# Kernel tuning notes

Hardware: AMD Instinct MI355X
Metric: run time of the kernel (lower is better)

Reference implementation:

```python
import jax, jax.numpy as jnp
import numpy as np

N, E, D, D_OUT = 100000, 3200000, 64, 64
EPS = 1e-5


def setup_inputs() -> dict:
    key = jax.random.key(0)
    ks = jax.random.split(key, 16)
    s = 1.0 / np.sqrt(D)
    inp = {
        "x": jax.random.normal(ks[0], (N, D), dtype=jnp.float32),
        "edge_index": jax.random.randint(ks[1], (2, E), 0, N, dtype=jnp.int64),
        # layer 1: GCNConv weight/bias, fc weight/bias, BN gamma/beta
        "W1": jax.random.uniform(ks[2], (D, D), jnp.float32, -s, s),
        "b1": jnp.zeros((D,), jnp.float32),
        "fw1": jax.random.uniform(ks[3], (D, D), jnp.float32, -s, s),
        "fb1": jax.random.uniform(ks[4], (D,), jnp.float32, -s, s),
        "g1": jnp.ones((D,), jnp.float32),
        "bt1": jnp.zeros((D,), jnp.float32),
        # layer 2
        "W2": jax.random.uniform(ks[5], (D, D), jnp.float32, -s, s),
        "b2": jnp.zeros((D,), jnp.float32),
        "fw2": jax.random.uniform(ks[6], (D, D_OUT), jnp.float32, -s, s),
        "fb2": jax.random.uniform(ks[7], (D_OUT,), jnp.float32, -s, s),
        "g2": jnp.ones((D_OUT,), jnp.float32),
        "bt2": jnp.zeros((D_OUT,), jnp.float32),
    }
    return inp


def _gcn_conv(x, W, b, src, dst, dinv):
    # x' = X W, then symmetric-normalized scatter-add aggregation (self loops included)
    h = x @ W                                   # [N, D]
    msg = (dinv[src] * dinv[dst])[:, None] * h[src]  # [E+N, D]
    out = jax.ops.segment_sum(msg, dst, num_segments=N)
    return out + b


def _fc_bn_relu(x, fw, fb, g, bt):
    y = x @ fw + fb
    mu = jnp.mean(y, axis=0)
    var = jnp.mean((y - mu) ** 2, axis=0)  # biased var (torch BN training mode)
    y = (y - mu) * jax.lax.rsqrt(var + EPS) * g + bt
    return jax.nn.relu(y)


def reference(x, edge_index, W1, b1, fw1, fb1, g1, bt1, W2, b2, fw2, fb2, g2, bt2):
    loop = jnp.arange(N, dtype=edge_index.dtype)
    src = jnp.concatenate([edge_index[0], loop])  # add self loops
    dst = jnp.concatenate([edge_index[1], loop])
    deg = jax.ops.segment_sum(jnp.ones_like(dst, dtype=x.dtype), dst, num_segments=N)
    dinv = jax.lax.rsqrt(deg)  # deg >= 1 thanks to self loops

    h = _gcn_conv(x, W1, b1, src, dst, dinv)
    h = _fc_bn_relu(h, fw1, fb1, g1, bt1)
    h = _gcn_conv(h, W2, b2, src, dst, dinv)
    h = _fc_bn_relu(h, fw2, fb2, g2, bt2)
    return h
```

## Files before the change

### kernel.cpp

```cpp
#include <hip/hip_runtime.h>

#define N_NODES 100000
#define N_EDGES 3200000
#define D 64
#define EPS 1e-5f

#define BSHIFT 7
#define BNODES 128
#define NBUCK ((N_NODES + BNODES - 1) / BNODES)
#define P1_CHUNK 4096
#define NB_P1 ((N_EDGES + P1_CHUNK - 1) / P1_CHUNK)
#define SRC_MASK 0x1FFFFu
#define BCAP 4480
#define TBL_STRIDE 784

typedef _Float16 f16x8 __attribute__((ext_vector_type(8)));
typedef _Float16 half2v __attribute__((ext_vector_type(2)));
typedef unsigned int u32x4 __attribute__((ext_vector_type(4)));
typedef __attribute__((ext_vector_type(4))) float f32x4;

__device__ __forceinline__ unsigned short f2h(float f) {
  return __builtin_bit_cast(unsigned short, (_Float16)f);
}
__device__ __forceinline__ half2v u2h(unsigned int u) {
  return __builtin_bit_cast(half2v, u);
}
__device__ __forceinline__ unsigned int h2u(half2v h) {
  return __builtin_bit_cast(unsigned int, h);
}
__device__ __forceinline__ float2 hpair(unsigned int u) {
  half2v h = __builtin_bit_cast(half2v, u);
  return make_float2((float)h.x, (float)h.y);
}
__device__ __forceinline__ void addp(half2v a[4], uint4 u) {
  a[0] += u2h(u.x);
  a[1] += u2h(u.y);
  a[2] += u2h(u.z);
  a[3] += u2h(u.w);
}

__global__ __launch_bounds__(256) void combine_weights(
    const float* __restrict__ W1, const float* __restrict__ b1,
    const float* __restrict__ fw1, const float* __restrict__ fb1,
    const float* __restrict__ W2, const float* __restrict__ b2,
    const float* __restrict__ fw2, const float* __restrict__ fb2,
    unsigned int* __restrict__ WcB1, float* __restrict__ bc1,
    unsigned int* __restrict__ WcB2, float* __restrict__ bc2,
    float* __restrict__ stats) {
  if (blockIdx.x == 2) {
    if (threadIdx.x < 256) stats[threadIdx.x] = 0.0f;
    return;
  }
  const float* W  = blockIdx.x ? W2  : W1;
  const float* fw = blockIdx.x ? fw2 : fw1;
  const float* b  = blockIdx.x ? b2  : b1;
  const float* fb = blockIdx.x ? fb2 : fb1;
  unsigned int* WcB = blockIdx.x ? WcB2 : WcB1;
  float* bc = blockIdx.x ? bc2 : bc1;

  __shared__ float sW[64 * 64];
  __shared__ float sf[64 * 64];
  __shared__ float sC[64 * 64];
  for (int i = threadIdx.x; i < 4096; i += 256) { sW[i] = W[i]; sf[i] = fw[i]; }
  __syncthreads();
  for (int o = threadIdx.x; o < 4096; o += 256) {
    int i = o >> 6, j = o & 63;
    float acc = 0.f;
    #pragma unroll
    for (int k = 0; k < 64; ++k) acc += sW[i * 64 + k] * sf[k * 64 + j];
    sC[o] = acc;
  }
  __syncthreads();
  for (int o = threadIdx.x; o < 2048; o += 256) {
    int jj = o & 3, L = (o >> 2) & 63, kh = (o >> 8) & 1, nt = o >> 9;
    int k0 = (L >> 4) * 8 + jj * 2 + kh * 32;
    int n  = nt * 16 + (L & 15);
    unsigned int lo = f2h(sC[k0 * 64 + n]);
    unsigned int hi = f2h(sC[(k0 + 1) * 64 + n]);
    WcB[o] = (hi << 16) | lo;
  }
  if (threadIdx.x < 64) {
    int j = threadIdx.x;
    float acc = fb[j];
    #pragma unroll
    for (int k = 0; k < 64; ++k) acc += b[k] * sf[k * 64 + j];
    bc[j] = acc;
  }
}

__global__ __launch_bounds__(256) void pass1_sort(
    const int* __restrict__ src, const int* __restrict__ dst,
    unsigned int* __restrict__ stage, unsigned short* __restrict__ tbl) {
  __shared__ unsigned int hist[NBUCK];
  __shared__ unsigned int ts[256];
  __shared__ unsigned int sorted[P1_CHUNK];
  const int tid = threadIdx.x;
  const int e0 = blockIdx.x * P1_CHUNK;

  for (int b = tid; b < NBUCK; b += 256) hist[b] = 0;
  __syncthreads();

  int dreg[16];
  #pragma unroll
  for (int k = 0; k < 16; ++k) {
    int e = e0 + k * 256 + tid;
    int d = (e < N_EDGES) ? dst[e] : -1;
    dreg[k] = d;
    if (d >= 0) atomicAdd(&hist[((unsigned)d) >> BSHIFT], 1u);
  }
  __syncthreads();

  unsigned int v[4], run = 0;
  #pragma unroll
  for (int j = 0; j < 4; ++j) {
    int bk = 4 * tid + j;
    unsigned int h = (bk < NBUCK) ? hist[bk] : 0u;
    v[j] = run;
    run += h;
  }
  ts[tid] = run;
  __syncthreads();
  for (int o = 1; o < 256; o <<= 1) {
    unsigned int add = (tid >= o) ? ts[tid - o] : 0u;
    __syncthreads();
    ts[tid] += add;
    __syncthreads();
  }
  const unsigned int excl = ts[tid] - run;
  const unsigned int m = ts[255];
  unsigned short* trow = tbl + (size_t)blockIdx.x * TBL_STRIDE;
  #pragma unroll
  for (int j = 0; j < 4; ++j) {
    int bk = 4 * tid + j;
    if (bk < NBUCK) {
      unsigned int o = excl + v[j];
      hist[bk] = o;
      trow[bk] = (unsigned short)o;
    }
  }
  if (tid == 0) trow[NBUCK] = (unsigned short)m;
  __syncthreads();

  #pragma unroll
  for (int k = 0; k < 16; ++k) {
    int e = e0 + k * 256 + tid;
    int t = dreg[k];
    if (t >= 0) {
      unsigned int pos = atomicAdd(&hist[((unsigned)t) >> BSHIFT], 1u);
      sorted[pos] = (((unsigned)(t & (BNODES - 1))) << 17) | (unsigned)src[e];
    }
  }
  __syncthreads();

  unsigned int* so = stage + (size_t)blockIdx.x * P1_CHUNK;
  for (int i = tid; i < (int)m; i += 256) so[i] = sorted[i];
}

__global__ __launch_bounds__(512) void pass2_sort(
    const unsigned int* __restrict__ stage, const unsigned short* __restrict__ tbl,
    int* __restrict__ eSrc, int* __restrict__ off, int* __restrict__ edeg,
    float* __restrict__ dinv, const float* __restrict__ x,
    unsigned short* __restrict__ Xs) {
  __shared__ int spre[512];
  __shared__ int cnt[BNODES];
  __shared__ int ts[BNODES];
  __shared__ float dinvL[BNODES];
  __shared__ unsigned int raw[BCAP];
  __shared__ int sorted[BCAP];
  const int b = blockIdx.x, tid = threadIdx.x;
  const int n0 = b * BNODES;

  int base0 = 0, base1 = 0, len0 = 0, len1 = 0;
  {
    int s0 = 2 * tid, s1 = 2 * tid + 1;
    if (s0 < NB_P1) {
      const unsigned short* trow = tbl + (size_t)s0 * TBL_STRIDE;
      int o0 = trow[b], o1 = trow[b + 1];
      base0 = s0 * P1_CHUNK + o0;
      len0 = o1 - o0;
    }
    if (s1 < NB_P1) {
      const unsigned short* trow = tbl + (size_t)s1 * TBL_STRIDE;
      int o0 = trow[b], o1 = trow[b + 1];
      base1 = s1 * P1_CHUNK + o0;
      len1 = o1 - o0;
    }
  }
  if (tid < BNODES) cnt[tid] = 0;
  const int mylen = len0 + len1;
  spre[tid] = mylen;
  __syncthreads();
  for (int o = 1; o < 512; o <<= 1) {
    int add = (tid >= o) ? spre[tid - o] : 0;
    __syncthreads();
    spre[tid] += add;
    __syncthreads();
  }
  const int m = spre[511];
  const int pref = spre[tid] - mylen;

  for (int j = 0; j < len0; ++j) {
    unsigned int p = stage[base0 + j];
    raw[pref + j] = p;
    atomicAdd(&cnt[p >> 17], 1);
  }
  for (int j = 0; j < len1; ++j) {
    unsigned int p = stage[base1 + j];
    raw[pref + len0 + j] = p;
    atomicAdd(&cnt[p >> 17], 1);
  }
  __syncthreads();

  int v = 0;
  if (tid < BNODES) { v = cnt[tid]; ts[tid] = v; }
  __syncthreads();
  for (int o = 1; o < BNODES; o <<= 1) {
    int add = (tid >= o && tid < BNODES) ? ts[tid - o] : 0;
    __syncthreads();
    if (tid < BNODES) ts[tid] += add;
    __syncthreads();
  }
  if (tid < BNODES) {
    int excl = ts[tid] - v;
    int node = n0 + tid;
    float dv = rsqrtf((float)v + 1.0f);
    dinvL[tid] = dv;
    if (node < N_NODES) {
      off[node]  = b * BCAP + excl;
      edeg[node] = v;
      dinv[node] = dv;
    }
    cnt[tid] = excl;
  }
  __syncthreads();

  for (int i = tid; i < m; i += 512) {
    unsigned int p = raw[i];
    int pos = atomicAdd(&cnt[p >> 17], 1);
    if (pos < BCAP) sorted[pos] = (int)(p & SRC_MASK);
  }
  __syncthreads();

  int* out = eSrc + (size_t)b * BCAP;
  for (int i = tid; i < m; i += 512) out[i] = sorted[i];

  const int rows = min(BNODES, N_NODES - n0);
  for (int i = tid; i < rows * 64; i += 512) {
    int r = i >> 6;
    size_t g = (size_t)(n0 + r) * 64 + (i & 63);
    Xs[g] = f2h(dinvL[r] * x[g]);
  }
}

__global__ __launch_bounds__(256) void agg_csr(
    const int* __restrict__ off, const int* __restrict__ edeg,
    const int* __restrict__ eSrc, const unsigned short* __restrict__ Xs,
    const float* __restrict__ dinv, unsigned short* __restrict__ agg) {
  const int wv = (blockIdx.x * 256 + threadIdx.x) >> 6;
  const int lane = threadIdx.x & 63;
  const int half = lane >> 5;
  const int l32 = lane & 31;
  const int grp = l32 >> 3;
  const int sub = lane & 7;
  const int node = wv * 2 + half;
  if (node >= N_NODES) return;

  const int s0 = off[node];
  const int deg = edeg[node];
  const float dvf = dinv[node];
  const uint4* XsV = (const uint4*)Xs;

  int eidx = node;
  if (deg > 0) {
    int li = (l32 < deg) ? l32 : deg - 1;
    eidx = __builtin_nontemporal_load(&eSrc[s0 + li]);
  }

  half2v acc[4];
  {
    uint4 u = XsV[(size_t)node * 8 + sub];
    if (l32 >= 8) { u.x = 0; u.y = 0; u.z = 0; u.w = 0; }
    acc[0] = u2h(u.x);
    acc[1] = u2h(u.y);
    acc[2] = u2h(u.z);
    acc[3] = u2h(u.w);
  }

  uint4 g[8];
  #pragma unroll
  for (int j = 0; j < 8; ++j) {
    int srcn = __shfl(eidx, half * 32 + j * 4 + grp, 64);
    g[j] = XsV[(size_t)srcn * 8 + sub];
  }
  #pragma unroll
  for (int j = 0; j < 8; ++j) {
    uint4 u = g[j];
    if (j * 4 + grp >= deg) { u.x = 0; u.y = 0; u.z = 0; u.w = 0; }
    addp(acc, u);
  }

  if (deg > 32) {
    const int lim = deg - 1;
    for (int e = 32; e < deg; e += 4) {
      int ee = e + grp;
      int srcn = __builtin_nontemporal_load(&eSrc[s0 + min(ee, lim)]);
      uint4 u = XsV[(size_t)srcn * 8 + sub];
      if (ee > lim) { u.x = 0; u.y = 0; u.z = 0; u.w = 0; }
      addp(acc, u);
    }
  }

  #pragma unroll
  for (int mk = 8; mk <= 16; mk <<= 1) {
    #pragma unroll
    for (int i = 0; i < 4; ++i)
      acc[i] += u2h(__shfl_xor(h2u(acc[i]), mk, 64));
  }

  if (l32 < 8) {
    _Float16 dh = (_Float16)dvf;
    half2v d2 = {dh, dh};
    u32x4 o;
    o.x = h2u(acc[0] * d2);
    o.y = h2u(acc[1] * d2);
    o.z = h2u(acc[2] * d2);
    o.w = h2u(acc[3] * d2);
    __builtin_nontemporal_store(o, (u32x4*)(agg + (size_t)node * 64 + sub * 8));
  }
}

__global__ __launch_bounds__(256) void gemm_stats(
    const unsigned short* __restrict__ A, const unsigned int* __restrict__ WcB,
    const float* __restrict__ bc, unsigned short* __restrict__ Yb,
    float* __restrict__ colsum, float* __restrict__ colsq) {
  const int tid = threadIdx.x;
  const int L = tid & 63, wv = tid >> 6;
  const int quad = L >> 4, l16 = L & 15;

  const f16x8* Wv = (const f16x8*)WcB;
  f16x8 bfr[4][2];
  #pragma unroll
  for (int nt = 0; nt < 4; ++nt)
    #pragma unroll
    for (int kh = 0; kh < 2; ++kh)
      bfr[nt][kh] = Wv[(nt * 2 + kh) * 64 + L];
  float bcv[4];
  #pragma unroll
  for (int nt = 0; nt < 4; ++nt) bcv[nt] = bc[nt * 16 + l16];

  const f16x8* Av = (const f16x8*)A;
  float psum[4] = {0.f, 0.f, 0.f, 0.f}, psq[4] = {0.f, 0.f, 0.f, 0.f};

  #pragma unroll
  for (int loop = 0; loop < 2; ++loop) {
    const int rowbase = blockIdx.x * 128 + loop * 64 + wv * 16;
    const int m = min(rowbase + l16, N_NODES - 1);
    f16x8 a0 = Av[(size_t)m * 8 + quad];
    f16x8 a1 = Av[(size_t)m * 8 + 4 + quad];
    #pragma unroll
    for (int nt = 0; nt < 4; ++nt) {
      f32x4 acc = {0.f, 0.f, 0.f, 0.f};
      acc = __builtin_amdgcn_mfma_f32_16x16x32_f16(a0, bfr[nt][0], acc, 0, 0, 0);
      acc = __builtin_amdgcn_mfma_f32_16x16x32_f16(a1, bfr[nt][1], acc, 0, 0, 0);
      #pragma unroll
      for (int r = 0; r < 4; ++r) {
        int row = rowbase + quad * 4 + r;
        if (row < N_NODES) {
          float y = acc[r] + bcv[nt];
          Yb[(size_t)row * 64 + nt * 16 + l16] = f2h(y);
          psum[nt] += y;
          psq[nt] += y * y;
        }
      }
    }
  }

  #pragma unroll
  for (int nt = 0; nt < 4; ++nt) {
    psum[nt] += __shfl_xor(psum[nt], 16, 64);
    psum[nt] += __shfl_xor(psum[nt], 32, 64);
    psq[nt]  += __shfl_xor(psq[nt], 16, 64);
    psq[nt]  += __shfl_xor(psq[nt], 32, 64);
  }
  __shared__ float rsum[4][64];
  __shared__ float rsq[4][64];
  if (L < 16) {
    #pragma unroll
    for (int nt = 0; nt < 4; ++nt) {
      rsum[wv][nt * 16 + L] = psum[nt];
      rsq[wv][nt * 16 + L]  = psq[nt];
    }
  }
  __syncthreads();
  if (tid < 64) {
    float s = rsum[0][tid] + rsum[1][tid] + rsum[2][tid] + rsum[3][tid];
    float q = rsq[0][tid] + rsq[1][tid] + rsq[2][tid] + rsq[3][tid];
    atomicAdd(&colsum[tid], s);
    atomicAdd(&colsq[tid], q);
  }
}

__global__ __launch_bounds__(256) void prescale_y(
    const unsigned short* __restrict__ Yin, unsigned short* __restrict__ Xout,
    const float* __restrict__ dinv,
    const float* __restrict__ colsum, const float* __restrict__ colsq,
    const float* __restrict__ g, const float* __restrict__ bt) {
  __shared__ float sa[64], sc[64];
  if (threadIdx.x < 64) {
    int j = threadIdx.x;
    float mu = colsum[j] * (1.0f / N_NODES);
    float var = colsq[j] * (1.0f / N_NODES) - mu * mu;
    float s = rsqrtf(var + EPS) * g[j];
    sa[j] = s;
    sc[j] = bt[j] - mu * s;
  }
  __syncthreads();
  int idx = blockIdx.x * blockDim.x + threadIdx.x;
  if (idx < N_NODES * 8) {
    int r = idx >> 3, c0 = (idx & 7) * 8;
    float dv = dinv[r];
    uint4 u = ((const uint4*)Yin)[idx];
    float2 p0 = hpair(u.x), p1 = hpair(u.y), p2 = hpair(u.z), p3 = hpair(u.w);
    p0.x = dv * fmaxf(fmaf(p0.x, sa[c0    ], sc[c0    ]), 0.f);
    p0.y = dv * fmaxf(fmaf(p0.y, sa[c0 + 1], sc[c0 + 1]), 0.f);
    p1.x = dv * fmaxf(fmaf(p1.x, sa[c0 + 2], sc[c0 + 2]), 0.f);
    p1.y = dv * fmaxf(fmaf(p1.y, sa[c0 + 3], sc[c0 + 3]), 0.f);
    p2.x = dv * fmaxf(fmaf(p2.x, sa[c0 + 4], sc[c0 + 4]), 0.f);
    p2.y = dv * fmaxf(fmaf(p2.y, sa[c0 + 5], sc[c0 + 5]), 0.f);
    p3.x = dv * fmaxf(fmaf(p3.x, sa[c0 + 6], sc[c0 + 6]), 0.f);
    p3.y = dv * fmaxf(fmaf(p3.y, sa[c0 + 7], sc[c0 + 7]), 0.f);
    uint4 o;
    o.x = ((unsigned)f2h(p0.y) << 16) | f2h(p0.x);
    o.y = ((unsigned)f2h(p1.y) << 16) | f2h(p1.x);
    o.z = ((unsigned)f2h(p2.y) << 16) | f2h(p2.x);
    o.w = ((unsigned)f2h(p3.y) << 16) | f2h(p3.x);
    ((uint4*)Xout)[idx] = o;
  }
}

__global__ __launch_bounds__(256) void final_norm(
    const unsigned short* __restrict__ Yb, float* __restrict__ out,
    const float* __restrict__ colsum, const float* __restrict__ colsq,
    const float* __restrict__ g, const float* __restrict__ bt) {
  __shared__ float sa[64], sc[64];
  if (threadIdx.x < 64) {
    int j = threadIdx.x;
    float mu = colsum[j] * (1.0f / N_NODES);
    float var = colsq[j] * (1.0f / N_NODES) - mu * mu;
    float s = rsqrtf(var + EPS) * g[j];
    sa[j] = s;
    sc[j] = bt[j] - mu * s;
  }
  __syncthreads();
  int idx = blockIdx.x * blockDim.x + threadIdx.x;
  if (idx < N_NODES * 8) {
    int c0 = (idx & 7) * 8;
    uint4 u = ((const uint4*)Yb)[idx];
    float2 p0 = hpair(u.x), p1 = hpair(u.y), p2 = hpair(u.z), p3 = hpair(u.w);
    float4 o0, o1;
    o0.x = fmaxf(fmaf(p0.x, sa[c0    ], sc[c0    ]), 0.f);
    o0.y = fmaxf(fmaf(p0.y, sa[c0 + 1], sc[c0 + 1]), 0.f);
    o0.z = fmaxf(fmaf(p1.x, sa[c0 + 2], sc[c0 + 2]), 0.f);
    o0.w = fmaxf(fmaf(p1.y, sa[c0 + 3], sc[c0 + 3]), 0.f);
    o1.x = fmaxf(fmaf(p2.x, sa[c0 + 4], sc[c0 + 4]), 0.f);
    o1.y = fmaxf(fmaf(p2.y, sa[c0 + 5], sc[c0 + 5]), 0.f);
    o1.z = fmaxf(fmaf(p3.x, sa[c0 + 6], sc[c0 + 6]), 0.f);
    o1.w = fmaxf(fmaf(p3.y, sa[c0 + 7], sc[c0 + 7]), 0.f);
    ((float4*)out)[idx * 2] = o0;
    ((float4*)out)[idx * 2 + 1] = o1;
  }
}

extern "C" void kernel_launch(void* const* d_in, const int* in_sizes, int n_in,
                              void* d_out, int out_size, void* d_ws, size_t ws_size,
                              hipStream_t stream) {
  const float* x   = (const float*)d_in[0];
  const int*   src = (const int*)d_in[1];
  const int*   dst = src + N_EDGES;
  const float* W1  = (const float*)d_in[2];
  const float* b1  = (const float*)d_in[3];
  const float* fw1 = (const float*)d_in[4];
  const float* fb1 = (const float*)d_in[5];
  const float* g1  = (const float*)d_in[6];
  const float* bt1 = (const float*)d_in[7];
  const float* W2  = (const float*)d_in[8];
  const float* b2  = (const float*)d_in[9];
  const float* fw2 = (const float*)d_in[10];
  const float* fb2 = (const float*)d_in[11];
  const float* g2  = (const float*)d_in[12];
  const float* bt2 = (const float*)d_in[13];

  float* out = (float*)d_out;

  unsigned char* w = (unsigned char*)d_ws;
  unsigned int*   stage = (unsigned int*)w;
  unsigned short* aggb  = (unsigned short*)w;
  size_t ofs = ((size_t)NB_P1 * P1_CHUNK * 4 + 255) & ~(size_t)255;
  float*          dinv  = (float*)(w + ofs);
  unsigned short* XsYb  = (unsigned short*)(dinv + N_NODES);
  int*            eSrc  = (int*)(XsYb + (size_t)N_NODES * D);
  int*            off   = eSrc + (size_t)NBUCK * BCAP;
  int*            edeg  = off + N_NODES;
  unsigned short* tbl   = (unsigned short*)(edeg + N_NODES);
  unsigned int* WcB1 = (unsigned int*)(tbl + (size_t)NB_P1 * TBL_STRIDE);
  float* bc1  = (float*)(WcB1 + 2048);
  unsigned int* WcB2 = (unsigned int*)(bc1 + 64);
  float* bc2  = (float*)(WcB2 + 2048);
  float* sum1 = bc2 + 64;
  float* sq1  = sum1 + 64;
  float* sum2 = sq1 + 64;
  float* sq2  = sum2 + 64;

  const int nv = N_NODES * 8;
  const int nagg = (N_NODES + 7) / 8;
  dim3 blk(256);

  combine_weights<<<3, blk, 0, stream>>>(W1, b1, fw1, fb1, W2, b2, fw2, fb2,
                                         WcB1, bc1, WcB2, bc2, sum1);
  pass1_sort<<<NB_P1, blk, 0, stream>>>(src, dst, stage, tbl);
  pass2_sort<<<NBUCK, 512, 0, stream>>>(stage, tbl, eSrc, off, edeg, dinv, x, XsYb);
  agg_csr<<<nagg, blk, 0, stream>>>(off, edeg, eSrc, XsYb, dinv, aggb);
  gemm_stats<<<(N_NODES + 127) / 128, blk, 0, stream>>>(aggb, WcB1, bc1, XsYb, sum1, sq1);
  prescale_y<<<(nv + 255) / 256, blk, 0, stream>>>(XsYb, XsYb, dinv, sum1, sq1, g1, bt1);
  agg_csr<<<nagg, blk, 0, stream>>>(off, edeg, eSrc, XsYb, dinv, aggb);
  gemm_stats<<<(N_NODES + 127) / 128, blk, 0, stream>>>(aggb, WcB2, bc2, XsYb, sum2, sq2);
  final_norm<<<(nv + 255) / 256, blk, 0, stream>>>(XsYb, out, sum2, sq2, g2, bt2);
}
```

Before: 324.6 us.

## Use wave-shuffle scans in sort passes, vectorize prescale, split aggregation launches

Replaces the shared-memory Hillis-Steele prefix scans in both sort passes with wavefront shuffle scans plus a small cross-wave combine, removing many block-wide barriers. Unrolls the stage-read loops in pass2 by four and vectorizes the x-to-half prescale with float4 loads and ushort4 stores. Splits each aggregation launch into two half-node launches through a new base offset, which adds launch overhead and may only change cache locality.

Result: no change. 328.0 us (+1.1%).

```diff
diff --git a/kernel.cpp b/kernel.cpp
--- a/kernel.cpp
+++ b/kernel.cpp
@@ -92,9 +92,10 @@
     const int* __restrict__ src, const int* __restrict__ dst,
     unsigned int* __restrict__ stage, unsigned short* __restrict__ tbl) {
   __shared__ unsigned int hist[NBUCK];
-  __shared__ unsigned int ts[256];
+  __shared__ unsigned int wsum4[4];
   __shared__ unsigned int sorted[P1_CHUNK];
   const int tid = threadIdx.x;
+  const int wvid = tid >> 6, ln = tid & 63;
   const int e0 = blockIdx.x * P1_CHUNK;
 
   for (int b = tid; b < NBUCK; b += 256) hist[b] = 0;
@@ -118,16 +119,23 @@
     v[j] = run;
     run += h;
   }
-  ts[tid] = run;
-  __syncthreads();
-  for (int o = 1; o < 256; o <<= 1) {
-    unsigned int add = (tid >= o) ? ts[tid - o] : 0u;
-    __syncthreads();
-    ts[tid] += add;
-    __syncthreads();
-  }
-  const unsigned int excl = ts[tid] - run;
-  const unsigned int m = ts[255];
+  unsigned int inc = run;
+  #pragma unroll
+  for (int o = 1; o < 64; o <<= 1) {
+    unsigned int t = __shfl_up(inc, o, 64);
+    if (ln >= o) inc += t;
+  }
+  if (ln == 63) wsum4[wvid] = inc;
+  __syncthreads();
+  unsigned int wbase = 0, mtot = 0;
+  #pragma unroll
+  for (int k = 0; k < 4; ++k) {
+    unsigned int s = wsum4[k];
+    mtot += s;
+    if (k < wvid) wbase += s;
+  }
+  const unsigned int excl = wbase + inc - run;
+  const unsigned int m = mtot;
   unsigned short* trow = tbl + (size_t)blockIdx.x * TBL_STRIDE;
   #pragma unroll
   for (int j = 0; j < 4; ++j) {
@@ -161,13 +169,14 @@
     int* __restrict__ eSrc, int* __restrict__ off, int* __restrict__ edeg,
     float* __restrict__ dinv, const float* __restrict__ x,
     unsigned short* __restrict__ Xs) {
-  __shared__ int spre[512];
   __shared__ int cnt[BNODES];
-  __shared__ int ts[BNODES];
+  __shared__ int wsum8[8];
+  __shared__ int csum2[2];
   __shared__ float dinvL[BNODES];
   __shared__ unsigned int raw[BCAP];
   __shared__ int sorted[BCAP];
   const int b = blockIdx.x, tid = threadIdx.x;
+  const int wvid = tid >> 6, ln = tid & 63;
   const int n0 = b * BNODES;
 
   int base0 = 0, base1 = 0, len0 = 0, len1 = 0;
@@ -188,40 +197,72 @@
   }
   if (tid < BNODES) cnt[tid] = 0;
   const int mylen = len0 + len1;
-  spre[tid] = mylen;
-  __syncthreads();
-  for (int o = 1; o < 512; o <<= 1) {
-    int add = (tid >= o) ? spre[tid - o] : 0;
-    __syncthreads();
-    spre[tid] += add;
-    __syncthreads();
-  }
-  const int m = spre[511];
-  const int pref = spre[tid] - mylen;
-
-  for (int j = 0; j < len0; ++j) {
-    unsigned int p = stage[base0 + j];
-    raw[pref + j] = p;
-    atomicAdd(&cnt[p >> 17], 1);
-  }
-  for (int j = 0; j < len1; ++j) {
-    unsigned int p = stage[base1 + j];
-    raw[pref + len0 + j] = p;
-    atomicAdd(&cnt[p >> 17], 1);
-  }
-  __syncthreads();
-
-  int v = 0;
-  if (tid < BNODES) { v = cnt[tid]; ts[tid] = v; }
-  __syncthreads();
-  for (int o = 1; o < BNODES; o <<= 1) {
-    int add = (tid >= o && tid < BNODES) ? ts[tid - o] : 0;
-    __syncthreads();
-    if (tid < BNODES) ts[tid] += add;
-    __syncthreads();
-  }
+
+  int inc = mylen;
+  #pragma unroll
+  for (int o = 1; o < 64; o <<= 1) {
+    int t = __shfl_up(inc, o, 64);
+    if (ln >= o) inc += t;
+  }
+  if (ln == 63) wsum8[wvid] = inc;
+  __syncthreads();
+  int wbase = 0, mtot = 0;
+  #pragma unroll
+  for (int k = 0; k < 8; ++k) {
+    int s = wsum8[k];
+    mtot += s;
+    if (k < wvid) wbase += s;
+  }
+  const int m = mtot;
+  const int pref = wbase + inc - mylen;
+
+  {
+    int j = 0;
+    for (; j + 4 <= len0; j += 4) {
+      unsigned int p0 = stage[base0 + j],     p1 = stage[base0 + j + 1];
+      unsigned int p2 = stage[base0 + j + 2], p3 = stage[base0 + j + 3];
+      raw[pref + j] = p0; raw[pref + j + 1] = p1;
+      raw[pref + j + 2] = p2; raw[pref + j + 3] = p3;
+      atomicAdd(&cnt[p0 >> 17], 1); atomicAdd(&cnt[p1 >> 17], 1);
+      atomicAdd(&cnt[p2 >> 17], 1); atomicAdd(&cnt[p3 >> 17], 1);
+    }
+    for (; j < len0; ++j) {
+      unsigned int p = stage[base0 + j];
+      raw[pref + j] = p;
+      atomicAdd(&cnt[p >> 17], 1);
+    }
+  }
+  {
+    const int pb = pref + len0;
+    int j = 0;
+    for (; j + 4 <= len1; j += 4) {
+      unsigned int p0 = stage[base1 + j],     p1 = stage[base1 + j + 1];
+      unsigned int p2 = stage[base1 + j + 2], p3 = stage[base1 + j + 3];
+      raw[pb + j] = p0; raw[pb + j + 1] = p1;
+      raw[pb + j + 2] = p2; raw[pb + j + 3] = p3;
+      atomicAdd(&cnt[p0 >> 17], 1); atomicAdd(&cnt[p1 >> 17], 1);
+      atomicAdd(&cnt[p2 >> 17], 1); atomicAdd(&cnt[p3 >> 17], 1);
+    }
+    for (; j < len1; ++j) {
+      unsigned int p = stage[base1 + j];
+      raw[pb + j] = p;
+      atomicAdd(&cnt[p >> 17], 1);
+    }
+  }
+  __syncthreads();
+
+  int v = (tid < BNODES) ? cnt[tid] : 0;
+  int cin = v;
+  #pragma unroll
+  for (int o = 1; o < 64; o <<= 1) {
+    int t = __shfl_up(cin, o, 64);
+    if (ln >= o) cin += t;
+  }
+  if (tid < BNODES && ln == 63) csum2[wvid] = cin;
+  __syncthreads();
   if (tid < BNODES) {
-    int excl = ts[tid] - v;
+    int incl = cin + ((wvid == 1) ? csum2[0] : 0);
+    int excl = incl - v;
     int node = n0 + tid;
     float dv = rsqrtf((float)v + 1.0f);
     dinvL[tid] = dv;
@@ -245,24 +286,31 @@
   for (int i = tid; i < m; i += 512) out[i] = sorted[i];
 
   const int rows = min(BNODES, N_NODES - n0);
-  for (int i = tid; i < rows * 64; i += 512) {
-    int r = i >> 6;
-    size_t g = (size_t)(n0 + r) * 64 + (i & 63);
-    Xs[g] = f2h(dinvL[r] * x[g]);
+  for (int i = tid; i < rows * 16; i += 512) {
+    int r = i >> 4, c = i & 15;
+    float4 xv = ((const float4*)x)[(size_t)(n0 + r) * 16 + c];
+    float dv = dinvL[r];
+    ushort4 o;
+    o.x = f2h(dv * xv.x);
+    o.y = f2h(dv * xv.y);
+    o.z = f2h(dv * xv.z);
+    o.w = f2h(dv * xv.w);
+    ((ushort4*)Xs)[(size_t)(n0 + r) * 16 + c] = o;
   }
 }
 
 __global__ __launch_bounds__(256) void agg_csr(
     const int* __restrict__ off, const int* __restrict__ edeg,
     const int* __restrict__ eSrc, const unsigned short* __restrict__ Xs,
-    const float* __restrict__ dinv, unsigned short* __restrict__ agg) {
+    const float* __restrict__ dinv, unsigned short* __restrict__ agg,
+    int nbase) {
   const int wv = (blockIdx.x * 256 + threadIdx.x) >> 6;
   const int lane = threadIdx.x & 63;
   const int half = lane >> 5;
   const int l32 = lane & 31;
   const int grp = l32 >> 3;
   const int sub = lane & 7;
-  const int node = wv * 2 + half;
+  const int node = nbase + wv * 2 + half;
   if (node >= N_NODES) return;
 
   const int s0 = off[node];
@@ -512,17 +560,19 @@
   float* sq2  = sum2 + 64;
 
   const int nv = N_NODES * 8;
-  const int nagg = (N_NODES + 7) / 8;
+  const int nagg2 = 6250;
   dim3 blk(256);
 
   combine_weights<<<3, blk, 0, stream>>>(W1, b1, fw1, fb1, W2, b2, fw2, fb2,
                                          WcB1, bc1, WcB2, bc2, sum1);
   pass1_sort<<<NB_P1, blk, 0, stream>>>(src, dst, stage, tbl);
   pass2_sort<<<NBUCK, 512, 0, stream>>>(stage, tbl, eSrc, off, edeg, dinv, x, XsYb);
-  agg_csr<<<nagg, blk, 0, stream>>>(off, edeg, eSrc, XsYb, dinv, aggb);
+  agg_csr<<<nagg2, blk, 0, stream>>>(off, edeg, eSrc, XsYb, dinv, aggb, 0);
+  agg_csr<<<nagg2, blk, 0, stream>>>(off, edeg, eSrc, XsYb, dinv, aggb, 50000);
   gemm_stats<<<(N_NODES + 127) / 128, blk, 0, stream>>>(aggb, WcB1, bc1, XsYb, sum1, sq1);
   prescale_y<<<(nv + 255) / 256, blk, 0, stream>>>(XsYb, XsYb, dinv, sum1, sq1, g1, bt1);
-  agg_csr<<<nagg, blk, 0, stream>>>(off, edeg, eSrc, XsYb, dinv, aggb);
+  agg_csr<<<nagg2, blk, 0, stream>>>(off, edeg, eSrc, XsYb, dinv, aggb, 0);
+  agg_csr<<<nagg2, blk, 0, stream>>>(off, edeg, eSrc, XsYb, dinv, aggb, 50000);
   gemm_stats<<<(N_NODES + 127) / 128, blk, 0, stream>>>(aggb, WcB2, bc2, XsYb, sum2, sq2);
   final_norm<<<(nv + 255) / 256, blk, 0, stream>>>(XsYb, out, sum2, sq2, g2, bt2);
 }
```
